# Kernel optimization log

Hardware: AMD Instinct MI355X
Metric: run time of the kernel (lower is better)

## Reference

```python
import jax, jax.numpy as jnp
import numpy as np

L, H, DH, D, F, BLK, VOCAB = 2, 16, 128, 2048, 8192, 64, 32000
B, S, R = 16, 77, 16
LORA_SCALE = 32.0 / 16.0  # alpha / r

# standard bitsandbytes NF4 codebook
NF4 = jnp.array([-1.0, -0.6961928009986877, -0.5250730514526367,
                 -0.39491748809814453, -0.28444138169288635, -0.18477343022823334,
                 -0.09105003625154495, 0.0, 0.07958029955625534, 0.16093020141124725,
                 0.24611230194568634, 0.33791524171829224, 0.44070982933044434,
                 0.5626170039176941, 0.723855197429657, 1.0], dtype=jnp.float32)


def setup_inputs() -> dict:
    key = jax.random.key(0)
    ks = jax.random.split(key, 24)
    n = lambda k, sh, s=0.02: jax.random.normal(k, sh, jnp.float32) * s
    u = lambda k, sh: jax.random.uniform(k, sh, dtype=jnp.float32) * 0.02
    ri = lambda k, sh, hi: jax.random.randint(k, sh, 0, hi, jnp.int32)
    return {
        "input_ids": ri(ks[0], (B, S), VOCAB),
        "attention_mask": jnp.ones((B, S), jnp.int32),
        "embed": n(ks[1], (VOCAB, D)),
        "ln_attn": jnp.ones((L, D), jnp.float32),
        "ln_mlp": jnp.ones((L, D), jnp.float32),
        "ln_final": jnp.ones((D,), jnp.float32),
        "qkv_codes": ri(ks[2], (L, 3, D, D), 16),
        "qkv_absmax": u(ks[3], (L, 3, D, D // BLK)),
        "qkv_A": n(ks[4], (L, 3, R, D)),
        "qkv_B": n(ks[5], (L, 3, D, R), 0.01),
        "o_codes": ri(ks[6], (L, D, D), 16),
        "o_absmax": u(ks[7], (L, D, D // BLK)),
        "o_A": n(ks[8], (L, R, D)),
        "o_B": n(ks[9], (L, D, R), 0.01),
        "gu_codes": ri(ks[10], (L, 2, F, D), 16),
        "gu_absmax": u(ks[11], (L, 2, F, D // BLK)),
        "gu_A": n(ks[12], (L, 2, R, D)),
        "gu_B": n(ks[13], (L, 2, F, R), 0.01),
        "down_codes": ri(ks[14], (L, D, F), 16),
        "down_absmax": u(ks[15], (L, D, F // BLK)),
        "down_A": n(ks[16], (L, R, F)),
        "down_B": n(ks[17], (L, D, R), 0.01),
    }


def _rmsnorm(x, w, eps=1e-6):
    return x * jax.lax.rsqrt(jnp.mean(x * x, axis=-1, keepdims=True) + eps) * w


def _dequant(codes, absmax):
    # codes: (out, cin) ints in [0,16); absmax: (out, cin//BLK) blockwise scales
    out, cin = codes.shape
    w = NF4[codes].reshape(out, cin // BLK, BLK) * absmax[..., None]
    return w.reshape(out, cin)


def _qlora(x, codes, absmax, A, Bm):
    # NF4 dequant base matmul + rank-R LoRA delta (eval mode, no dropout)
    W = _dequant(codes, absmax)
    return x @ W.T + LORA_SCALE * ((x @ A.T) @ Bm.T)


def _rope_cache(seq):
    inv = 1.0 / (10000.0 ** (jnp.arange(0, DH, 2, dtype=jnp.float32) / DH))
    f = jnp.arange(seq, dtype=jnp.float32)[:, None] * inv  # (S, DH/2)
    emb = jnp.concatenate([f, f], axis=-1)                 # (S, DH)
    return jnp.cos(emb), jnp.sin(emb)


def _rope(x, cos, sin):
    # x: (B, H, S, DH), llama-style rotate_half
    x1, x2 = jnp.split(x, 2, axis=-1)
    return x * cos + jnp.concatenate([-x2, x1], axis=-1) * sin


def _forward(input_ids, attention_mask, embed, ln_attn, ln_mlp, ln_final,
             qkv_codes, qkv_absmax, qkv_A, qkv_B,
             o_codes, o_absmax, o_A, o_B,
             gu_codes, gu_absmax, gu_A, gu_B,
             down_codes, down_absmax, down_A, down_B):
    b, s = input_ids.shape
    h = embed[input_ids]                                    # (B, S, D)
    cos, sin = _rope_cache(s)
    pad = attention_mask.astype(bool)[:, None, None, :]     # (B,1,1,S)
    mask = pad & jnp.tril(jnp.ones((s, s), bool))
    inv_sqrt_dh = np.float32(1.0 / np.sqrt(DH))
    for l in range(L):
        x = _rmsnorm(h, ln_attn[l])
        q, k, v = [_qlora(x, qkv_codes[l, i], qkv_absmax[l, i], qkv_A[l, i], qkv_B[l, i])
                   .reshape(b, s, H, DH).transpose(0, 2, 1, 3) for i in range(3)]
        q, k = _rope(q, cos, sin), _rope(k, cos, sin)
        scores = jnp.einsum('bhqd,bhkd->bhqk', q, k) * inv_sqrt_dh
        attn = jax.nn.softmax(jnp.where(mask, scores, -1e9), axis=-1)
        o = jnp.einsum('bhqk,bhkd->bhqd', attn, v).transpose(0, 2, 1, 3).reshape(b, s, D)
        h = h + _qlora(o, o_codes[l], o_absmax[l], o_A[l], o_B[l])
        x = _rmsnorm(h, ln_mlp[l])
        g = _qlora(x, gu_codes[l, 0], gu_absmax[l, 0], gu_A[l, 0], gu_B[l, 0])
        up = _qlora(x, gu_codes[l, 1], gu_absmax[l, 1], gu_A[l, 1], gu_B[l, 1])
        h = h + _qlora(jax.nn.silu(g) * up,
                       down_codes[l], down_absmax[l], down_A[l], down_B[l])
    h = _rmsnorm(h, ln_final)
    lengths = attention_mask.sum(axis=1) - 1                # last non-pad token index
    return h[jnp.arange(b), lengths]                        # (B, D)


def reference(input_ids, attention_mask, embed, ln_attn, ln_mlp, ln_final,
              qkv_codes, qkv_absmax, qkv_A, qkv_B,
              o_codes, o_absmax, o_A, o_B,
              gu_codes, gu_absmax, gu_A, gu_B,
              down_codes, down_absmax, down_A, down_B):
    return _forward(input_ids, attention_mask, embed, ln_attn, ln_mlp, ln_final,
                    qkv_codes, qkv_absmax, qkv_A, qkv_B,
                    o_codes, o_absmax, o_A, o_B,
                    gu_codes, gu_absmax, gu_A, gu_B,
                    down_codes, down_absmax, down_A, down_B)
```

## Files before the change

### kernel.cpp

```cpp
#include <hip/hip_runtime.h>
#include <cstdint>
#include <cstddef>

#define M_TOK   1232
#define M_PAD   1280
#define D_MODEL 2048
#define F_FFN   8192
#define SEQ     77
#define BATCH   16
#define NHEAD   16
#define LRANK   16
#define NLAYER  2
#define ATILE   16
#define MWB     512

typedef short bf16x8 __attribute__((ext_vector_type(8)));
typedef float f32x4  __attribute__((ext_vector_type(4)));

__device__ __constant__ float NF4C[16] = {
  -1.0f, -0.6961928009986877f, -0.5250730514526367f, -0.39491748809814453f,
  -0.28444138169288635f, -0.18477343022823334f, -0.09105003625154495f, 0.0f,
  0.07958029955625534f, 0.16093020141124725f, 0.24611230194568634f,
  0.33791524171829224f, 0.44070982933044434f, 0.5626170039176941f,
  0.723855197429657f, 1.0f };

__device__ inline unsigned short f2b(float f) {
  unsigned u = __builtin_bit_cast(unsigned, f);
  u += 0x7FFFu + ((u >> 16) & 1u);
  return (unsigned short)(u >> 16);
}
__device__ inline float b2f(unsigned short s) {
  return __builtin_bit_cast(float, ((unsigned)s) << 16);
}

__global__ __launch_bounds__(256) void mat_w(
    const int* __restrict__ C, const float* __restrict__ AM,
    unsigned short* __restrict__ W, int K, long total8, int ilv)
{
  __shared__ float tb[16];
  if (threadIdx.x < 16) tb[threadIdx.x] = NF4C[threadIdx.x];
  __syncthreads();
  const int KB = K >> 6;
  for (long i = (long)blockIdx.x * 256 + threadIdx.x; i < total8;
       i += (long)gridDim.x * 256) {
    long e = i << 3;
    int rd = (int)(e / K), k = (int)(e - (long)rd * K);
    int srcn = ilv ? ((rd & 1) * F_FFN + (rd >> 1)) : rd;
    float am = AM[(size_t)srcn * KB + (k >> 6)];
    const int4* cp = (const int4*)(C + (size_t)srcn * K + k);
    int4 a = cp[0], b = cp[1];
    uint4 o;
    o.x = (unsigned)f2b(tb[a.x] * am) | ((unsigned)f2b(tb[a.y] * am) << 16);
    o.y = (unsigned)f2b(tb[a.z] * am) | ((unsigned)f2b(tb[a.w] * am) << 16);
    o.z = (unsigned)f2b(tb[b.x] * am) | ((unsigned)f2b(tb[b.y] * am) << 16);
    o.w = (unsigned)f2b(tb[b.z] * am) | ((unsigned)f2b(tb[b.w] * am) << 16);
    *(uint4*)(W + e) = o;
  }
}

__global__ __launch_bounds__(256, 2) void gemm_bf(
    const unsigned short* __restrict__ X, const unsigned short* __restrict__ W,
    float* __restrict__ O, int mb, int N, int K, int acc_mode, int splitk,
    const float* __restrict__ T, const float* __restrict__ Bm, int sh, int nr,
    int gum, unsigned short* __restrict__ GB,
    const int* __restrict__ C2, const float* __restrict__ AM2,
    unsigned short* __restrict__ W2, int K2, long total8_2, int ilv2, int Ggemm)
{
  __shared__ __align__(16) unsigned short xs[128 * 64];
  __shared__ __align__(16) unsigned short ws[128 * 64];

  int tid = threadIdx.x;

  if ((int)blockIdx.x >= Ggemm) {
    if (total8_2 > 0) {
      float* tb = (float*)xs;
      if (tid < 16) tb[tid] = NF4C[tid];
      __syncthreads();
      int nblk2 = gridDim.x - Ggemm;
      const int KB2 = K2 >> 6;
      for (long i = (long)((int)blockIdx.x - Ggemm) * 256 + tid; i < total8_2;
           i += (long)nblk2 * 256) {
        long e = i << 3;
        int rd = (int)(e / K2), k = (int)(e - (long)rd * K2);
        int srcn = ilv2 ? ((rd & 1) * F_FFN + (rd >> 1)) : rd;
        float am = AM2[(size_t)srcn * KB2 + (k >> 6)];
        const int4* cp = (const int4*)(C2 + (size_t)srcn * K2 + k);
        int4 a = cp[0], b = cp[1];
        uint4 o;
        o.x = (unsigned)f2b(tb[a.x] * am) | ((unsigned)f2b(tb[a.y] * am) << 16);
        o.y = (unsigned)f2b(tb[a.z] * am) | ((unsigned)f2b(tb[a.w] * am) << 16);
        o.z = (unsigned)f2b(tb[b.x] * am) | ((unsigned)f2b(tb[b.y] * am) << 16);
        o.w = (unsigned)f2b(tb[b.z] * am) | ((unsigned)f2b(tb[b.w] * am) << 16);
        *(uint4*)(W2 + e) = o;
      }
    }
    return;
  }

  int nwg = Ggemm;
  int q8 = nwg >> 3, r8 = nwg & 7;
  int xcd = blockIdx.x & 7, pos = blockIdx.x >> 3;
  int wgid = (xcd < r8) ? (xcd * (q8 + 1) + pos)
                        : (r8 * (q8 + 1) + (xcd - r8) * q8 + pos);
  int nb = N >> 7;
  int per = mb * nb;
  int slice = wgid / per; int rem = wgid - slice * per;
  int nblk = rem / mb, mblk = rem - nblk * mb;
  int row0 = mblk << 7, col0 = nblk << 7;
  int KBtot = K >> 6, kcnt = KBtot / splitk, kbeg = slice * kcnt;

  int wave = tid >> 6, lane = tid & 63;
  int fr = lane & 15, fg = lane >> 4, s7 = fr & 7;
  int wm = (wave >> 1) * 64, wn = (wave & 1) * 64;
  int xg = lane >> 3;
  int xcol = (((lane & 7) ^ (xg & 7)) << 3);

  const unsigned short* Xbase = X + (size_t)row0 * K + (size_t)kbeg * 64;
  const unsigned short* Wbase = W + (size_t)col0 * K + (size_t)kbeg * 64;

  f32x4 accm[4][4];
  #pragma unroll
  for (int i = 0; i < 4; ++i)
    #pragma unroll
    for (int j = 0; j < 4; ++j) accm[i][j] = (f32x4){0.f, 0.f, 0.f, 0.f};

  auto stage = [&](int t) {
    const unsigned short* xb = Xbase + (size_t)t * 64;
    const unsigned short* wb = Wbase + (size_t)t * 64;
    #pragma unroll
    for (int p2 = 0; p2 < 4; ++p2) {
      int c = wave * 4 + p2;
      const unsigned short* gp = xb + (size_t)(c * 8 + xg) * K + xcol;
      __builtin_amdgcn_global_load_lds(
          (const __attribute__((address_space(1))) unsigned int*)gp,
          (__attribute__((address_space(3))) unsigned int*)(xs + c * 512),
          16, 0, 0);
    }
    #pragma unroll
    for (int p2 = 0; p2 < 4; ++p2) {
      int c = wave * 4 + p2;
      const unsigned short* gp = wb + (size_t)(c * 8 + xg) * K + xcol;
      __builtin_amdgcn_global_load_lds(
          (const __attribute__((address_space(1))) unsigned int*)gp,
          (__attribute__((address_space(3))) unsigned int*)(ws + c * 512),
          16, 0, 0);
    }
  };
  auto compute = [&]() {
    bf16x8 b0[4], b1[4];
    #pragma unroll
    for (int ni = 0; ni < 4; ++ni) {
      const unsigned short* wr = ws + (wn + ni * 16 + fr) * 64;
      b0[ni] = *(const bf16x8*)(wr + ((fg ^ s7) << 3));
      b1[ni] = *(const bf16x8*)(wr + (((4 | fg) ^ s7) << 3));
    }
    #pragma unroll
    for (int mi = 0; mi < 4; ++mi) {
      const unsigned short* xr = xs + (wm + mi * 16 + fr) * 64;
      bf16x8 a0 = *(const bf16x8*)(xr + ((fg ^ s7) << 3));
      bf16x8 a1 = *(const bf16x8*)(xr + (((4 | fg) ^ s7) << 3));
      #pragma unroll
      for (int ni = 0; ni < 4; ++ni) {
        accm[mi][ni] = __builtin_amdgcn_mfma_f32_16x16x32_bf16(
            a0, b0[ni], accm[mi][ni], 0, 0, 0);
        accm[mi][ni] = __builtin_amdgcn_mfma_f32_16x16x32_bf16(
            a1, b1[ni], accm[mi][ni], 0, 0, 0);
      }
    }
  };

  stage(0);
  for (int t = 0; t < kcnt; ++t) {
    __syncthreads();
    compute();
    if (t + 1 < kcnt) {
      __syncthreads();
      stage(t + 1);
    }
  }

  if (gum) {
    float* Tt = (float*)&xs[0];
    float* Bt = (float*)&ws[0];
    __syncthreads();
    for (int idx = tid; idx < 128 * 32; idx += 256) {
      int rr = idx >> 5, c = idx & 31;
      int gm = row0 + rr;
      Tt[idx] = (gm < M_TOK) ? T[(size_t)gm * 32 + c] : 0.f;
    }
    for (int idx = tid; idx < 128 * 16; idx += 256) {
      int rr = idx >> 4, c = idx & 15;
      int type = rr & 1, nrow = (col0 + rr) >> 1;
      Bt[idx] = Bm[((size_t)type * F_FFN + nrow) * LRANK + c];
    }
    __syncthreads();
    #pragma unroll
    for (int mi = 0; mi < 4; ++mi)
      #pragma unroll
      for (int ni = 0; ni < 4; ++ni) {
        int gm0 = row0 + wm + mi * 16 + fg * 4;
        int gnl = wn + ni * 16 + fr;
        #pragma unroll
        for (int r = 0; r < 4; ++r) {
          int gm = gm0 + r;
          float vv = accm[mi][ni][r];
          const float* tr = Tt + (wm + mi * 16 + fg * 4 + r) * 32 + ((gnl & 1) << 4);
          const float* br = Bt + gnl * 16;
          float s = 0.f;
          #pragma unroll
          for (int c = 0; c < 16; ++c) s += tr[c] * br[c];
          vv += 2.0f * s;
          float prt = __shfl_xor(vv, 1);
          if (gm < M_TOK && !(fr & 1)) {
            float sig = 1.0f / (1.0f + expf(-vv));
            GB[(size_t)gm * F_FFN + ((col0 + gnl) >> 1)] = f2b(vv * sig * prt);
          }
        }
      }
    return;
  }

  float* Tt = (float*)&xs[0];
  float* Bt = (float*)&ws[0];
  if (T) {
    __syncthreads();
    int toff = (col0 >> sh) << 4;
    for (int idx = tid; idx < 128 * 16; idx += 256) {
      int rr = idx >> 4, c = idx & 15;
      int gm = row0 + rr;
      Tt[idx] = (gm < M_TOK) ? T[(size_t)gm * nr + toff + c] : 0.f;
      Bt[idx] = Bm[(size_t)(col0 + rr) * LRANK + c];
    }
    __syncthreads();
  }

  #pragma unroll
  for (int mi = 0; mi < 4; ++mi)
    #pragma unroll
    for (int ni = 0; ni < 4; ++ni) {
      int gm0 = row0 + wm + mi * 16 + fg * 4;
      int gnl = wn + ni * 16 + fr;
      int gn = col0 + gnl;
      #pragma unroll
      for (int r = 0; r < 4; ++r) {
        int gm = gm0 + r;
        if (gm < M_TOK) {
          size_t idx = (size_t)gm * N + gn;
          float vv = accm[mi][ni][r];
          if (T) {
            const float* tr = Tt + (wm + mi * 16 + fg * 4 + r) * 16;
            const float* br = Bt + gnl * 16;
            float s = 0.f;
            #pragma unroll
            for (int c = 0; c < 16; ++c) s += tr[c] * br[c];
            vv += 2.0f * s;
          }
          if (splitk > 1)       atomicAdd(&O[idx], vv);
          else if (acc_mode)    O[idx] += vv;
          else                  O[idx] = vv;
        }
      }
    }
}

__global__ __launch_bounds__(256) void lora1(
    const unsigned short* __restrict__ X, const float* __restrict__ A,
    float* __restrict__ T, int K)
{
  int m0 = blockIdx.x * 4, bi = blockIdx.y, nmat = gridDim.y;
  int g = threadIdx.x >> 4, l16 = threadIdx.x & 15;
  const float* ar = A + (size_t)bi * LRANK * K + (size_t)g * K;
  const unsigned short* x0 = X + (size_t)m0 * K;
  float s0 = 0.f, s1 = 0.f, s2 = 0.f, s3 = 0.f;
  for (int kk = l16 * 4; kk < K; kk += 64) {
    float4 av = *(const float4*)(ar + kk);
    ushort4 v0 = *(const ushort4*)(x0 + kk);
    ushort4 v1 = *(const ushort4*)(x0 + K + kk);
    ushort4 v2 = *(const ushort4*)(x0 + 2 * K + kk);
    ushort4 v3 = *(const ushort4*)(x0 + 3 * K + kk);
    s0 += b2f(v0.x)*av.x + b2f(v0.y)*av.y + b2f(v0.z)*av.z + b2f(v0.w)*av.w;
    s1 += b2f(v1.x)*av.x + b2f(v1.y)*av.y + b2f(v1.z)*av.z + b2f(v1.w)*av.w;
    s2 += b2f(v2.x)*av.x + b2f(v2.y)*av.y + b2f(v2.z)*av.z + b2f(v2.w)*av.w;
    s3 += b2f(v3.x)*av.x + b2f(v3.y)*av.y + b2f(v3.z)*av.z + b2f(v3.w)*av.w;
  }
  #pragma unroll
  for (int off = 8; off; off >>= 1) {
    s0 += __shfl_down(s0, off, 16);
    s1 += __shfl_down(s1, off, 16);
    s2 += __shfl_down(s2, off, 16);
    s3 += __shfl_down(s3, off, 16);
  }
  if (l16 == 0) {
    size_t base = ((size_t)m0 * nmat + bi) * LRANK + g;
    size_t rs = (size_t)nmat * LRANK;
    T[base] = s0; T[base + rs] = s1; T[base + 2*rs] = s2; T[base + 3*rs] = s3;
  }
}

__global__ __launch_bounds__(256) void lora2(
    float* __restrict__ O, const float* __restrict__ T,
    const float* __restrict__ Bm, int N, int sh, int nr)
{
  int m0 = blockIdx.y * 8;
  int n = blockIdx.x * 256 + threadIdx.x;
  __shared__ float ts[8 * 48];
  for (int i = threadIdx.x; i < 8 * nr; i += 256)
    ts[(i / nr) * 48 + (i % nr)] = T[(size_t)(m0 + i / nr) * nr + (i % nr)];
  __syncthreads();
  const float4* br = (const float4*)(Bm + (size_t)n * LRANK);
  float4 b0 = br[0], b1 = br[1], b2 = br[2], b3 = br[3];
  int toff = ((n >> sh) << 4);
  #pragma unroll
  for (int mi = 0; mi < 8; ++mi) {
    const float* tsb = ts + mi * 48 + toff;
    float s = b0.x*tsb[0] + b0.y*tsb[1] + b0.z*tsb[2] + b0.w*tsb[3]
            + b1.x*tsb[4] + b1.y*tsb[5] + b1.z*tsb[6] + b1.w*tsb[7]
            + b2.x*tsb[8] + b2.y*tsb[9] + b2.z*tsb[10] + b2.w*tsb[11]
            + b3.x*tsb[12] + b3.y*tsb[13] + b3.z*tsb[14] + b3.w*tsb[15];
    O[(size_t)(m0 + mi) * N + n] += 2.0f * s;
  }
}

__global__ __launch_bounds__(256) void rmsnorm_k(
    const float* __restrict__ H, const float* __restrict__ W,
    unsigned short* __restrict__ X, int D)
{
  int m = blockIdx.x;
  const float* hr = H + (size_t)m * D;
  float s = 0.f;
  for (int i = threadIdx.x; i < D; i += 256) { float v = hr[i]; s += v * v; }
  __shared__ float red[4];
  #pragma unroll
  for (int off = 32; off; off >>= 1) s += __shfl_down(s, off, 64);
  if ((threadIdx.x & 63) == 0) red[threadIdx.x >> 6] = s;
  __syncthreads();
  float tot = red[0] + red[1] + red[2] + red[3];
  float inv = rsqrtf(tot / (float)D + 1e-6f);
  for (int i = threadIdx.x; i < D; i += 256)
    X[(size_t)m * D + i] = f2b(hr[i] * inv * W[i]);
}

__global__ void rope_table(float* __restrict__ cosT, float* __restrict__ sinT)
{
  int idx = blockIdx.x * 64 + threadIdx.x;
  if (idx >= SEQ * 64) return;
  int s = idx >> 6, j = idx & 63;
  float inv = powf(10000.0f, -(float)(2 * j) / 128.0f);
  float f = (float)s * inv;
  cosT[idx] = cosf(f);
  sinT[idx] = sinf(f);
}

__global__ __launch_bounds__(256) void attn_k(
    const float* __restrict__ QKV, const int* __restrict__ amask,
    const float* __restrict__ cosT, const float* __restrict__ sinT,
    unsigned short* __restrict__ O)
{
  int bh = blockIdx.x, it = blockIdx.y;
  int b = bh >> 4, h = bh & (NHEAD - 1);
  const int STR = 3 * D_MODEL;
  __shared__ float ks[SEQ * 132];
  __shared__ float qs[ATILE * 132];
  __shared__ float sc[ATILE * 80];
  __shared__ int am[SEQ];
  const float scale = 0.08838834764831845f;

  const float* Kb = QKV + (size_t)(b * SEQ) * STR + D_MODEL + h * 128;
  for (int idx = threadIdx.x; idx < SEQ * 16; idx += 256) {
    int j = idx >> 4, dq = (idx & 15) << 2;
    float4 a = *(const float4*)(Kb + (size_t)j * STR + dq);
    float4 bb = *(const float4*)(Kb + (size_t)j * STR + dq + 64);
    float4 c4 = *(const float4*)(cosT + j * 64 + dq);
    float4 s4 = *(const float4*)(sinT + j * 64 + dq);
    float* kr = ks + j * 132 + dq;
    kr[0] = a.x*c4.x - bb.x*s4.x; kr[1] = a.y*c4.y - bb.y*s4.y;
    kr[2] = a.z*c4.z - bb.z*s4.z; kr[3] = a.w*c4.w - bb.w*s4.w;
    kr[64] = bb.x*c4.x + a.x*s4.x; kr[65] = bb.y*c4.y + a.y*s4.y;
    kr[66] = bb.z*c4.z + a.z*s4.z; kr[67] = bb.w*c4.w + a.w*s4.w;
  }
  const float* Qb = QKV + (size_t)(b * SEQ) * STR + h * 128;
  for (int idx = threadIdx.x; idx < ATILE * 16; idx += 256) {
    int il = idx >> 4, dq = (idx & 15) << 2;
    int i = it * ATILE + il;
    if (i < SEQ) {
      float4 a = *(const float4*)(Qb + (size_t)i * STR + dq);
      float4 bb = *(const float4*)(Qb + (size_t)i * STR + dq + 64);
      float4 c4 = *(const float4*)(cosT + i * 64 + dq);
      float4 s4 = *(const float4*)(sinT + i * 64 + dq);
      float* qr = qs + il * 132 + dq;
      qr[0] = a.x*c4.x - bb.x*s4.x; qr[1] = a.y*c4.y - bb.y*s4.y;
      qr[2] = a.z*c4.z - bb.z*s4.z; qr[3] = a.w*c4.w - bb.w*s4.w;
      qr[64] = bb.x*c4.x + a.x*s4.x; qr[65] = bb.y*c4.y + a.y*s4.y;
      qr[66] = bb.z*c4.z + a.z*s4.z; qr[67] = bb.w*c4.w + a.w*s4.w;
    }
  }
  for (int j = threadIdx.x; j < SEQ; j += 256) am[j] = amask[b * SEQ + j];
  __syncthreads();

  int wave = threadIdx.x >> 6, lane = threadIdx.x & 63;
  #pragma unroll
  for (int r = 0; r < 4; ++r) {
    int il = wave * 4 + r;
    int i = it * ATILE + il;
    if (i < SEQ) {
      const float4* qr = (const float4*)(qs + il * 132);
      int j1 = lane, j2 = lane + 64;
      float v1 = -1e9f, v2 = -1e9f;
      if (j1 <= i && am[j1]) {
        const float4* kr = (const float4*)(ks + j1 * 132);
        float s = 0.f;
        #pragma unroll 8
        for (int d = 0; d < 32; ++d) {
          float4 a = qr[d], c = kr[d];
          s += a.x*c.x + a.y*c.y + a.z*c.z + a.w*c.w;
        }
        v1 = s * scale;
      }
      if (j2 < SEQ && j2 <= i && am[j2]) {
        const float4* kr = (const float4*)(ks + j2 * 132);
        float s = 0.f;
        #pragma unroll 8
        for (int d = 0; d < 32; ++d) {
          float4 a = qr[d], c = kr[d];
          s += a.x*c.x + a.y*c.y + a.z*c.z + a.w*c.w;
        }
        v2 = s * scale;
      }
      float mx = fmaxf(v1, v2);
      #pragma unroll
      for (int off = 32; off; off >>= 1) mx = fmaxf(mx, __shfl_xor(mx, off));
      float e1 = __expf(v1 - mx);
      float e2 = (j2 < SEQ) ? __expf(v2 - mx) : 0.f;
      float sum = e1 + e2;
      #pragma unroll
      for (int off = 32; off; off >>= 1) sum += __shfl_xor(sum, off);
      float inv = 1.0f / sum;
      sc[il * 80 + j1] = e1 * inv;
      if (j2 < SEQ) sc[il * 80 + j2] = e2 * inv;
    }
  }
  __syncthreads();

  const float* Vbase = QKV + (size_t)(b * SEQ) * STR + 2 * D_MODEL + h * 128;
  for (int idx = threadIdx.x; idx < ATILE * 32; idx += 256) {
    int il = idx >> 5, d4 = (idx & 31) << 2;
    int i = it * ATILE + il;
    if (i >= SEQ) continue;
    float4 acc = {0.f, 0.f, 0.f, 0.f};
    const float* sr = sc + il * 80;
    for (int j = 0; j < SEQ; ++j) {
      float pp = sr[j];
      float4 v = *(const float4*)(Vbase + (size_t)j * STR + d4);
      acc.x += pp * v.x; acc.y += pp * v.y; acc.z += pp * v.z; acc.w += pp * v.w;
    }
    unsigned short* op = O + (size_t)(b * SEQ + i) * D_MODEL + h * 128 + d4;
    op[0] = f2b(acc.x); op[1] = f2b(acc.y); op[2] = f2b(acc.z); op[3] = f2b(acc.w);
  }
}

__global__ void embed_gather(const float* __restrict__ E, const int* __restrict__ ids,
                             float* __restrict__ H)
{
  size_t idx = (size_t)blockIdx.x * 256 + threadIdx.x;
  int m = (int)(idx / D_MODEL);
  int n = (int)(idx % D_MODEL);
  H[idx] = E[(size_t)ids[m] * D_MODEL + n];
}

__global__ __launch_bounds__(256) void final_k(
    const float* __restrict__ H, const int* __restrict__ amask,
    const float* __restrict__ W, float* __restrict__ out)
{
  int b = blockIdx.x;
  __shared__ int len;
  if (threadIdx.x == 0) {
    int s = 0;
    for (int j = 0; j < SEQ; ++j) s += amask[b * SEQ + j];
    len = s - 1;
  }
  __syncthreads();
  const float* hr = H + ((size_t)(b * SEQ + len) * D_MODEL);
  float s = 0.f;
  for (int i = threadIdx.x; i < D_MODEL; i += 256) { float v = hr[i]; s += v * v; }
  __shared__ float red[4];
  #pragma unroll
  for (int off = 32; off; off >>= 1) s += __shfl_down(s, off, 64);
  if ((threadIdx.x & 63) == 0) red[threadIdx.x >> 6] = s;
  __syncthreads();
  float tot = red[0] + red[1] + red[2] + red[3];
  float inv = rsqrtf(tot / (float)D_MODEL + 1e-6f);
  for (int i = threadIdx.x; i < D_MODEL; i += 256)
    out[(size_t)b * D_MODEL + i] = hr[i] * inv * W[i];
}

extern "C" void kernel_launch(void* const* d_in, const int* in_sizes, int n_in,
                              void* d_out, int out_size, void* d_ws, size_t ws_size,
                              hipStream_t stream) {
  const int*   ids     = (const int*)d_in[0];
  const int*   amask   = (const int*)d_in[1];
  const float* embed   = (const float*)d_in[2];
  const float* ln_attn = (const float*)d_in[3];
  const float* ln_mlp  = (const float*)d_in[4];
  const float* ln_fin  = (const float*)d_in[5];
  const int*   qkvC    = (const int*)d_in[6];
  const float* qkvS    = (const float*)d_in[7];
  const float* qkvA    = (const float*)d_in[8];
  const float* qkvB    = (const float*)d_in[9];
  const int*   oC      = (const int*)d_in[10];
  const float* oS      = (const float*)d_in[11];
  const float* oA      = (const float*)d_in[12];
  const float* oB      = (const float*)d_in[13];
  const int*   guC     = (const int*)d_in[14];
  const float* guS     = (const float*)d_in[15];
  const float* guA     = (const float*)d_in[16];
  const float* guB     = (const float*)d_in[17];
  const int*   dnC     = (const int*)d_in[18];
  const float* dnS     = (const float*)d_in[19];
  const float* dnA     = (const float*)d_in[20];
  const float* dnB     = (const float*)d_in[21];
  float* out = (float*)d_out;

  const int M = M_TOK, Mp = M_PAD, D = D_MODEL, F = F_FFN, R = LRANK;
  float* p = (float*)d_ws;
  float* h    = p; p += (size_t)Mp * D;
  float* qkv  = p; p += (size_t)Mp * 3 * D;
  float* t    = p; p += (size_t)Mp * 48;
  float* cosT = p; p += SEQ * 64;
  float* sinT = p; p += SEQ * 64;
  unsigned short* xbf = (unsigned short*)p; p += (size_t)Mp * D / 2;
  unsigned short* gbf = (unsigned short*)p; p += (size_t)Mp * F / 2;
  unsigned short* wQ = (unsigned short*)p; p += (size_t)3 * D * D / 2;
  unsigned short* wO = (unsigned short*)p; p += (size_t)D * D / 2;
  unsigned short* wG = (unsigned short*)p; p += (size_t)2 * F * D / 2;
  unsigned short* wD = (unsigned short*)p; p += (size_t)D * F / 2;

  rope_table<<<(SEQ*64 + 63)/64, 64, 0, stream>>>(cosT, sinT);
  embed_gather<<<(M * D)/256, 256, 0, stream>>>(embed, ids, h);
  mat_w<<<2048, 256, 0, stream>>>(qkvC, qkvS, wQ, D, (long)3*D*D/8, 0);

  const int mb = Mp / 128;
  const int Gqkv = mb * (3*D/128);
  const int Go   = mb * (D/128) * 4;
  const int Ggu  = mb * (2*F/128);
  const int Gdn  = mb * (D/128) * 8;

  for (int l = 0; l < NLAYER; ++l) {
    rmsnorm_k<<<M, 256, 0, stream>>>(h, ln_attn + (size_t)l * D, xbf, D);
    lora1<<<dim3(M/4, 3), 256, 0, stream>>>(xbf, qkvA + (size_t)l*3*R*D, t, D);
    gemm_bf<<<Gqkv + MWB, 256, 0, stream>>>(
        xbf, wQ, qkv, mb, 3*D, D, 0, 1,
        t, qkvB + (size_t)l*3*D*R, 11, 48, 0, nullptr,
        oC + (size_t)l*D*D, oS + (size_t)l*D*(D/64), wO, D, (long)D*D/8, 0, Gqkv);
    attn_k<<<dim3(BATCH*NHEAD, (SEQ + ATILE - 1)/ATILE), 256, 0, stream>>>(
        qkv, amask, cosT, sinT, xbf);
    gemm_bf<<<Go + MWB, 256, 0, stream>>>(
        xbf, wO, h, mb, D, D, 1, 4, nullptr, nullptr, 0, 0, 0, nullptr,
        guC + (size_t)l*2*F*D, guS + (size_t)l*2*F*(D/64), wG, D, (long)2*F*D/8, 1, Go);
    lora1<<<dim3(M/4, 1), 256, 0, stream>>>(xbf, oA + (size_t)l*R*D, t, D);
    lora2<<<dim3(D/256, M/8), 256, 0, stream>>>(h, t, oB + (size_t)l*D*R, D, 11, 16);

    rmsnorm_k<<<M, 256, 0, stream>>>(h, ln_mlp + (size_t)l * D, xbf, D);
    lora1<<<dim3(M/4, 2), 256, 0, stream>>>(xbf, guA + (size_t)l*2*R*D, t, D);
    gemm_bf<<<Ggu + MWB, 256, 0, stream>>>(
        xbf, wG, nullptr, mb, 2*F, D, 0, 1,
        t, guB + (size_t)l*2*F*R, 0, 32, 1, gbf,
        dnC + (size_t)l*D*F, dnS + (size_t)l*D*(F/64), wD, F, (long)D*F/8, 0, Ggu);
    if (l + 1 < NLAYER) {
      gemm_bf<<<Gdn + MWB, 256, 0, stream>>>(
          gbf, wD, h, mb, D, F, 1, 8, nullptr, nullptr, 0, 0, 0, nullptr,
          qkvC + (size_t)(l+1)*3*D*D, qkvS + (size_t)(l+1)*3*D*(D/64),
          wQ, D, (long)3*D*D/8, 0, Gdn);
    } else {
      gemm_bf<<<Gdn, 256, 0, stream>>>(
          gbf, wD, h, mb, D, F, 1, 8, nullptr, nullptr, 0, 0, 0, nullptr,
          nullptr, nullptr, nullptr, D, 0, 0, Gdn);
    }
    lora1<<<dim3(M/4, 1), 256, 0, stream>>>(gbf, dnA + (size_t)l*R*F, t, F);
    lora2<<<dim3(D/256, M/8), 256, 0, stream>>>(h, t, dnB + (size_t)l*D*R, D, 11, 16);
  }
  final_k<<<BATCH, 256, 0, stream>>>(h, amask, ln_fin, out);
}
```

Measured before the change: 1.192 ms.

## Interleave dequant carry blocks with GEMM tiles and rebalance carry work

```diff
diff --git a/kernel.cpp b/kernel.cpp
--- a/kernel.cpp
+++ b/kernel.cpp
@@ -12,7 +12,6 @@
 #define LRANK   16
 #define NLAYER  2
 #define ATILE   16
-#define MWB     512
 
 typedef short bf16x8 __attribute__((ext_vector_type(8)));
 typedef float f32x4  __attribute__((ext_vector_type(4)));
@@ -33,29 +32,35 @@
   return __builtin_bit_cast(float, ((unsigned)s) << 16);
 }
 
-__global__ __launch_bounds__(256) void mat_w(
-    const int* __restrict__ C, const float* __restrict__ AM,
-    unsigned short* __restrict__ W, int K, long total8, int ilv)
-{
-  __shared__ float tb[16];
-  if (threadIdx.x < 16) tb[threadIdx.x] = NF4C[threadIdx.x];
-  __syncthreads();
-  const int KB = K >> 6;
-  for (long i = (long)blockIdx.x * 256 + threadIdx.x; i < total8;
-       i += (long)gridDim.x * 256) {
-    long e = i << 3;
-    int rd = (int)(e / K), k = (int)(e - (long)rd * K);
-    int srcn = ilv ? ((rd & 1) * F_FFN + (rd >> 1)) : rd;
-    float am = AM[(size_t)srcn * KB + (k >> 6)];
-    const int4* cp = (const int4*)(C + (size_t)srcn * K + k);
+__device__ inline void carry_body(const float* tb, long cid, long ncb, int tid,
+                                  const int* C2, const float* AM2,
+                                  unsigned short* W2, int K2, long beg8,
+                                  long cnt8, int ilv2) {
+  const int KB2 = K2 >> 6;
+  for (long i = cid * 256 + tid; i < cnt8; i += ncb * 256) {
+    long e = (beg8 + i) << 3;
+    int rd = (int)(e / K2), k = (int)(e - (long)rd * K2);
+    int srcn = ilv2 ? ((rd & 1) * F_FFN + (rd >> 1)) : rd;
+    float am = AM2[(size_t)srcn * KB2 + (k >> 6)];
+    const int4* cp = (const int4*)(C2 + (size_t)srcn * K2 + (k & (K2 - 1)));
     int4 a = cp[0], b = cp[1];
     uint4 o;
     o.x = (unsigned)f2b(tb[a.x] * am) | ((unsigned)f2b(tb[a.y] * am) << 16);
     o.y = (unsigned)f2b(tb[a.z] * am) | ((unsigned)f2b(tb[a.w] * am) << 16);
     o.z = (unsigned)f2b(tb[b.x] * am) | ((unsigned)f2b(tb[b.y] * am) << 16);
     o.w = (unsigned)f2b(tb[b.z] * am) | ((unsigned)f2b(tb[b.w] * am) << 16);
-    *(uint4*)(W + e) = o;
-  }
+    *(uint4*)(W2 + e) = o;
+  }
+}
+
+__global__ __launch_bounds__(256) void mat_w(
+    const int* __restrict__ C, const float* __restrict__ AM,
+    unsigned short* __restrict__ W, int K, long total8, int ilv)
+{
+  __shared__ float tb[16];
+  if (threadIdx.x < 16) tb[threadIdx.x] = NF4C[threadIdx.x];
+  __syncthreads();
+  carry_body(tb, blockIdx.x, gridDim.x, threadIdx.x, C, AM, W, K, 0, total8, ilv);
 }
 
 __global__ __launch_bounds__(256, 2) void gemm_bf(
@@ -64,42 +69,36 @@
     const float* __restrict__ T, const float* __restrict__ Bm, int sh, int nr,
     int gum, unsigned short* __restrict__ GB,
     const int* __restrict__ C2, const float* __restrict__ AM2,
-    unsigned short* __restrict__ W2, int K2, long total8_2, int ilv2, int Ggemm)
+    unsigned short* __restrict__ W2, int K2, long beg8, long cnt8, int ilv2,
+    int cpat, int Ggemm)
 {
   __shared__ __align__(16) unsigned short xs[128 * 64];
   __shared__ __align__(16) unsigned short ws[128 * 64];
 
   int tid = threadIdx.x;
-
-  if ((int)blockIdx.x >= Ggemm) {
-    if (total8_2 > 0) {
+  int bid = blockIdx.x;
+
+  int gemm_id = bid, cflag = 0; long cid = 0, ncb = 0;
+  if (cpat == 1) {
+    cflag = bid & 1; gemm_id = bid >> 1; cid = bid >> 1; ncb = gridDim.x >> 1;
+  } else if (cpat == 3) {
+    cflag = ((bid & 3) == 3); gemm_id = (bid >> 2) * 3 + (bid & 3);
+    cid = bid >> 2; ncb = gridDim.x >> 2;
+  }
+  if (cflag) {
+    if (cnt8 > 0) {
       float* tb = (float*)xs;
       if (tid < 16) tb[tid] = NF4C[tid];
       __syncthreads();
-      int nblk2 = gridDim.x - Ggemm;
-      const int KB2 = K2 >> 6;
-      for (long i = (long)((int)blockIdx.x - Ggemm) * 256 + tid; i < total8_2;
-           i += (long)nblk2 * 256) {
-        long e = i << 3;
-        int rd = (int)(e / K2), k = (int)(e - (long)rd * K2);
-        int srcn = ilv2 ? ((rd & 1) * F_FFN + (rd >> 1)) : rd;
-        float am = AM2[(size_t)srcn * KB2 + (k >> 6)];
-        const int4* cp = (const int4*)(C2 + (size_t)srcn * K2 + k);
-        int4 a = cp[0], b = cp[1];
-        uint4 o;
-        o.x = (unsigned)f2b(tb[a.x] * am) | ((unsigned)f2b(tb[a.y] * am) << 16);
-        o.y = (unsigned)f2b(tb[a.z] * am) | ((unsigned)f2b(tb[a.w] * am) << 16);
-        o.z = (unsigned)f2b(tb[b.x] * am) | ((unsigned)f2b(tb[b.y] * am) << 16);
-        o.w = (unsigned)f2b(tb[b.z] * am) | ((unsigned)f2b(tb[b.w] * am) << 16);
-        *(uint4*)(W2 + e) = o;
-      }
+      carry_body(tb, cid, ncb, tid, C2, AM2, W2, K2, beg8, cnt8, ilv2);
     }
     return;
   }
+  if (gemm_id >= Ggemm) return;
 
   int nwg = Ggemm;
   int q8 = nwg >> 3, r8 = nwg & 7;
-  int xcd = blockIdx.x & 7, pos = blockIdx.x >> 3;
+  int xcd = gemm_id & 7, pos = gemm_id >> 3;
   int wgid = (xcd < r8) ? (xcd * (q8 + 1) + pos)
                         : (r8 * (q8 + 1) + (xcd - r8) * q8 + pos);
   int nb = N >> 7;
@@ -220,9 +219,10 @@
     return;
   }
 
+  int doT = (T != nullptr) && (slice == 0);
   float* Tt = (float*)&xs[0];
   float* Bt = (float*)&ws[0];
-  if (T) {
+  if (doT) {
     __syncthreads();
     int toff = (col0 >> sh) << 4;
     for (int idx = tid; idx < 128 * 16; idx += 256) {
@@ -247,7 +247,7 @@
         if (gm < M_TOK) {
           size_t idx = (size_t)gm * N + gn;
           float vv = accm[mi][ni][r];
-          if (T) {
+          if (doT) {
             const float* tr = Tt + (wm + mi * 16 + fg * 4 + r) * 16;
             const float* br = Bt + gnl * 16;
             float s = 0.f;
@@ -354,15 +354,27 @@
 __global__ __launch_bounds__(256) void attn_k(
     const float* __restrict__ QKV, const int* __restrict__ amask,
     const float* __restrict__ cosT, const float* __restrict__ sinT,
-    unsigned short* __restrict__ O)
-{
-  int bh = blockIdx.x, it = blockIdx.y;
-  int b = bh >> 4, h = bh & (NHEAD - 1);
-  const int STR = 3 * D_MODEL;
+    unsigned short* __restrict__ O,
+    const int* __restrict__ C2, const float* __restrict__ AM2,
+    unsigned short* __restrict__ W2, long cnt8)
+{
   __shared__ float ks[SEQ * 132];
   __shared__ float qs[ATILE * 132];
   __shared__ float sc[ATILE * 80];
   __shared__ int am[SEQ];
+
+  if (blockIdx.y == 0) {
+    float* tb = ks;
+    if (threadIdx.x < 16) tb[threadIdx.x] = NF4C[threadIdx.x];
+    __syncthreads();
+    carry_body(tb, blockIdx.x, gridDim.x, threadIdx.x,
+               C2, AM2, W2, D_MODEL, 0, cnt8, 0);
+    return;
+  }
+
+  int bh = blockIdx.x, it = blockIdx.y - 1;
+  int b = bh >> 4, h = bh & (NHEAD - 1);
+  const int STR = 3 * D_MODEL;
   const float scale = 0.08838834764831845f;
 
   const float* Kb = QKV + (size_t)(b * SEQ) * STR + D_MODEL + h * 128;
@@ -539,41 +551,51 @@
   mat_w<<<2048, 256, 0, stream>>>(qkvC, qkvS, wQ, D, (long)3*D*D/8, 0);
 
   const int mb = Mp / 128;
-  const int Gqkv = mb * (3*D/128);
+  const int Gqkv = mb * (3*D/128) * 2;
   const int Go   = mb * (D/128) * 4;
   const int Ggu  = mb * (2*F/128);
   const int Gdn  = mb * (D/128) * 8;
+  const long guHalf = (long)F * D / 8;
 
   for (int l = 0; l < NLAYER; ++l) {
     rmsnorm_k<<<M, 256, 0, stream>>>(h, ln_attn + (size_t)l * D, xbf, D);
     lora1<<<dim3(M/4, 3), 256, 0, stream>>>(xbf, qkvA + (size_t)l*3*R*D, t, D);
-    gemm_bf<<<Gqkv + MWB, 256, 0, stream>>>(
-        xbf, wQ, qkv, mb, 3*D, D, 0, 1,
+    hipMemsetAsync(qkv, 0, (size_t)Mp * 3 * D * sizeof(float), stream);
+    gemm_bf<<<Gqkv * 2, 256, 0, stream>>>(
+        xbf, wQ, qkv, mb, 3*D, D, 0, 2,
         t, qkvB + (size_t)l*3*D*R, 11, 48, 0, nullptr,
-        oC + (size_t)l*D*D, oS + (size_t)l*D*(D/64), wO, D, (long)D*D/8, 0, Gqkv);
-    attn_k<<<dim3(BATCH*NHEAD, (SEQ + ATILE - 1)/ATILE), 256, 0, stream>>>(
-        qkv, amask, cosT, sinT, xbf);
-    gemm_bf<<<Go + MWB, 256, 0, stream>>>(
+        guC + (size_t)l*2*F*D, guS + (size_t)l*2*F*(D/64), wG, D,
+        0, guHalf, 1, 1, Gqkv);
+    attn_k<<<dim3(BATCH*NHEAD, (SEQ + ATILE - 1)/ATILE + 1), 256, 0, stream>>>(
+        qkv, amask, cosT, sinT, xbf,
+        oC + (size_t)l*D*D, oS + (size_t)l*D*(D/64), wO, (long)D*D/8);
+    gemm_bf<<<Go * 2, 256, 0, stream>>>(
         xbf, wO, h, mb, D, D, 1, 4, nullptr, nullptr, 0, 0, 0, nullptr,
-        guC + (size_t)l*2*F*D, guS + (size_t)l*2*F*(D/64), wG, D, (long)2*F*D/8, 1, Go);
+        guC + (size_t)l*2*F*D, guS + (size_t)l*2*F*(D/64), wG, D,
+        guHalf, guHalf, 1, 1, Go);
     lora1<<<dim3(M/4, 1), 256, 0, stream>>>(xbf, oA + (size_t)l*R*D, t, D);
     lora2<<<dim3(D/256, M/8), 256, 0, stream>>>(h, t, oB + (size_t)l*D*R, D, 11, 16);
 
     rmsnorm_k<<<M, 256, 0, stream>>>(h, ln_mlp + (size_t)l * D, xbf, D);
     lora1<<<dim3(M/4, 2), 256, 0, stream>>>(xbf, guA + (size_t)l*2*R*D, t, D);
-    gemm_bf<<<Ggu + MWB, 256, 0, stream>>>(
-        xbf, wG, nullptr, mb, 2*F, D, 0, 1,
-        t, guB + (size_t)l*2*F*R, 0, 32, 1, gbf,
-        dnC + (size_t)l*D*F, dnS + (size_t)l*D*(F/64), wD, F, (long)D*F/8, 0, Ggu);
+    {
+      int q = (Ggu + 2) / 3, G = 4 * q;
+      gemm_bf<<<G, 256, 0, stream>>>(
+          xbf, wG, nullptr, mb, 2*F, D, 0, 1,
+          t, guB + (size_t)l*2*F*R, 0, 32, 1, gbf,
+          dnC + (size_t)l*D*F, dnS + (size_t)l*D*(F/64), wD, F,
+          0, (long)D*F/8, 0, 3, Ggu);
+    }
     if (l + 1 < NLAYER) {
-      gemm_bf<<<Gdn + MWB, 256, 0, stream>>>(
+      int q = (Gdn + 2) / 3, G = 4 * q;
+      gemm_bf<<<G, 256, 0, stream>>>(
           gbf, wD, h, mb, D, F, 1, 8, nullptr, nullptr, 0, 0, 0, nullptr,
-          qkvC + (size_t)(l+1)*3*D*D, qkvS + (size_t)(l+1)*3*D*(D/64),
-          wQ, D, (long)3*D*D/8, 0, Gdn);
+          qkvC + (size_t)(l+1)*3*D*D, qkvS + (size_t)(l+1)*3*D*(D/64), wQ, D,
+          0, (long)3*D*D/8, 0, 3, Gdn);
     } else {
       gemm_bf<<<Gdn, 256, 0, stream>>>(
           gbf, wD, h, mb, D, F, 1, 8, nullptr, nullptr, 0, 0, 0, nullptr,
-          nullptr, nullptr, nullptr, D, 0, 0, Gdn);
+          nullptr, nullptr, nullptr, D, 0, 0, 0, 0, Gdn);
     }
     lora1<<<dim3(M/4, 1), 256, 0, stream>>>(gbf, dnA + (size_t)l*R*F, t, F);
     lora2<<<dim3(D/256, M/8), 256, 0, stream>>>(h, t, dnB + (size_t)l*D*R, D, 11, 16);
```

Measured after the change: 1.499 ms. 25.8% more time.
